# Kernel tuning notes

Measured on AMD Instinct MI355X. Metric: run time of the kernel, lower is better.

## Reference

```python
import jax, jax.numpy as jnp
import numpy as np

TAU_PLUS = 0.02
TAU_MINUS = 0.02
TAU_X = 0.101
A_TRIPLET = 0.0065
HOMEOSTATIC_RATE = 0.1
DT = 0.001
SPIKE_P = 0.05  # spike probability used to binarize inputs


def setup_inputs() -> dict:
    key = jax.random.key(0)
    k1, k2, k3 = jax.random.split(key, 3)
    B, P, Q, T = 16, 2048, 2048, 256
    pre_spikes = (jax.random.uniform(k1, (B, P, T)) < SPIKE_P).astype(jnp.float32)
    post_spikes = (jax.random.uniform(k2, (B, Q, T)) < SPIKE_P).astype(jnp.float32)
    weights = jax.random.normal(k3, (P, Q), dtype=jnp.float32) * 0.1
    meta_A_plus = jnp.float32(0.01)
    meta_A_minus = jnp.float32(0.012)
    return {"pre_spikes": pre_spikes, "post_spikes": post_spikes,
            "weights": weights, "meta_A_plus": meta_A_plus,
            "meta_A_minus": meta_A_minus}


def _traces(spikes_tbn, decay):
    """Trace value used at step t: x_t = decay * (x_{t-1} + s_{t-1}), x_0 = 0."""
    def step(carry, s):
        x = decay * carry          # decayed trace, used for this step's update
        return x + s, x            # spike added AFTER the update, per original
    init = jnp.zeros(spikes_tbn.shape[1:], spikes_tbn.dtype)
    _, xs = jax.lax.scan(step, init, spikes_tbn)
    return xs  # [T, B, N]


def reference(pre_spikes, post_spikes, weights, meta_A_plus, meta_A_minus):
    B, P, T = pre_spikes.shape
    exp_plus = jnp.exp(jnp.float32(-DT / TAU_PLUS))
    exp_minus = jnp.exp(jnp.float32(-DT / TAU_MINUS))
    exp_x = jnp.exp(jnp.float32(-DT / TAU_X))

    pre_t = jnp.transpose(pre_spikes, (2, 0, 1))    # [T, B, P]
    post_t = jnp.transpose(post_spikes, (2, 0, 1))  # [T, B, Q]

    x_pre = _traces(pre_t, exp_plus)     # [T, B, P]
    x_post = _traces(post_t, exp_minus)  # [T, B, Q]
    x_trip = _traces(post_t, exp_x)      # [T, B, Q]

    # Per-step outer products summed over time == one big contraction over (t, b).
    ltp = jnp.einsum('tbp,tbq->pq', x_pre, post_t) * meta_A_plus
    triplet = jnp.einsum('tbp,tbq->pq', x_pre, post_t * x_trip) * A_TRIPLET
    ltd = jnp.einsum('tbp,tbq->pq', pre_t, x_post) * meta_A_minus
    weight_updates = ltp + triplet - ltd

    # Homeostatic scaling (fresh module: activity history holds only this sample)
    current_activity = (pre_spikes.sum() + post_spikes.sum()) / (B * T)
    scaling_factor = jnp.sqrt(HOMEOSTATIC_RATE / (current_activity + 1e-6))

    updated_weights = weights + weight_updates * scaling_factor
    return jnp.clip(updated_weights, -2.0, 2.0)
```

## Files before the change

### kernel.cpp

```cpp
#include <hip/hip_runtime.h>

constexpr int TB = 16;
constexpr int NP = 2048;
constexpr int NQ = 2048;
constexpr int TT = 256;
constexpr int KH = TB * TT;
constexpr int KT = 2 * KH;

typedef unsigned short ushort_t;
typedef __attribute__((ext_vector_type(8))) __bf16 bf16x8;
typedef __attribute__((ext_vector_type(4))) float f32x4;

__device__ __forceinline__ ushort_t f2bf(float f) {
    unsigned u = __builtin_bit_cast(unsigned, f);
    u = (u + 0x7FFFu + ((u >> 16) & 1u)) >> 16;
    return (ushort_t)u;
}

union Pack16 { ushort_t u[16]; uint4 v[2]; };

constexpr float DF1 = 0.95122942450071400910f;
constexpr float DF2 = DF1 * DF1;
constexpr float DF4 = DF2 * DF2;
constexpr float DF8 = DF4 * DF4;
constexpr float DF16 = DF8 * DF8;
constexpr float DF32 = DF16 * DF16;
constexpr float DF64 = DF32 * DF32;
constexpr float DF128 = DF64 * DF64;

constexpr float DX1 = 0.99014786386058731819f;
constexpr float DX2 = DX1 * DX1;
constexpr float DX4 = DX2 * DX2;
constexpr float DX8 = DX4 * DX4;
constexpr float DX16 = DX8 * DX8;
constexpr float DX32 = DX16 * DX16;
constexpr float DX64 = DX32 * DX32;
constexpr float DX128 = DX64 * DX64;

template <int K>
__device__ __forceinline__ float seg_step(float b, float pw, int sl) {
    float t = __shfl_up(b, K, 64);
    return (sl >= K) ? fmaf(pw, t, b) : b;
}

__global__ __launch_bounds__(256, 1) void stage_traces(
    const float* __restrict__ pre, const float* __restrict__ post,
    const float* __restrict__ mApP, const float* __restrict__ mAmP,
    ushort_t* __restrict__ Ab, ushort_t* __restrict__ Bb,
    float* __restrict__ partials)
{
    const int tid  = threadIdx.x;
    const int lane = tid & 63;
    const int wv   = tid >> 6;
    const int sl   = lane & 15;
    const int seg  = lane >> 4;
    const int rowg = blockIdx.x * 16 + wv * 4 + seg;
    const bool isPre = rowg < TB * NP;
    const int m = isPre ? rowg : rowg - TB * NP;
    const int b = m >> 11;
    const int r = m & 2047;

    const float4* src = (const float4*)((isPre ? pre : post) + (size_t)m * TT);
    float f[16];
    #pragma unroll
    for (int j = 0; j < 4; ++j) {
        float4 u = src[sl * 4 + j];
        f[4 * j] = u.x; f[4 * j + 1] = u.y; f[4 * j + 2] = u.z; f[4 * j + 3] = u.w;
    }
    float cnt = 0.f;
    #pragma unroll
    for (int j = 0; j < 16; ++j) cnt += f[j];

    float Cf = 0.f;
    #pragma unroll
    for (int j = 0; j < 16; ++j) Cf = DF1 * (Cf + f[j]);
    float bs = Cf;
    bs = seg_step<1>(bs, DF16, sl);
    bs = seg_step<2>(bs, DF32, sl);
    bs = seg_step<4>(bs, DF64, sl);
    bs = seg_step<8>(bs, DF128, sl);
    float xinf = __shfl_up(bs, 1, 64);
    if (sl == 0) xinf = 0.f;

    float xf[16];
    {
        float x = xinf;
        #pragma unroll
        for (int j = 0; j < 16; ++j) { xf[j] = x; x = DF1 * (x + f[j]); }
    }

    Pack16 pa, pb;
    if (isPre) {
        #pragma unroll
        for (int j = 0; j < 16; ++j) {
            pa.u[j] = f2bf(xf[j]);
            pb.u[j] = (f[j] != 0.f) ? 0x3F80u : 0u;
        }
    } else {
        float Cx = 0.f;
        #pragma unroll
        for (int j = 0; j < 16; ++j) Cx = DX1 * (Cx + f[j]);
        float bx = Cx;
        bx = seg_step<1>(bx, DX16, sl);
        bx = seg_step<2>(bx, DX32, sl);
        bx = seg_step<4>(bx, DX64, sl);
        bx = seg_step<8>(bx, DX128, sl);
        float xint = __shfl_up(bx, 1, 64);
        if (sl == 0) xint = 0.f;

        const float Ap = *mApP;
        const float Am = *mAmP;
        float xt = xint;
        #pragma unroll
        for (int j = 0; j < 16; ++j) {
            pa.u[j] = (f[j] != 0.f) ? f2bf(fmaf(0.0065f, xt, Ap)) : 0u;
            pb.u[j] = f2bf(-Am * xf[j]);
            xt = DX1 * (xt + f[j]);
        }
    }

    ushort_t* o0 = (isPre ? Ab : Bb) + (size_t)r * KT + b * TT + sl * 16;
    *(uint4*)o0       = pa.v[0];
    *(uint4*)(o0 + 8) = pa.v[1];
    *(uint4*)(o0 + KH)     = pb.v[0];
    *(uint4*)(o0 + KH + 8) = pb.v[1];

    #pragma unroll
    for (int off = 32; off > 0; off >>= 1)
        cnt += __shfl_down(cnt, off, 64);
    __shared__ float wsum[4];
    if (lane == 0) wsum[wv] = cnt;
    __syncthreads();
    if (tid == 0) {
        float s = (wsum[0] + wsum[1]) + (wsum[2] + wsum[3]);
        atomicAdd(&partials[(blockIdx.x & 63) * 16], s);
    }
}

__device__ __forceinline__ void async16(const ushort_t* g, ushort_t* l) {
    __builtin_amdgcn_global_load_lds(
        (const __attribute__((address_space(1))) unsigned int*)g,
        (__attribute__((address_space(3))) unsigned int*)l,
        16, 0, 0);
}

__global__ __launch_bounds__(256, 2) void gemm_split(
    const ushort_t* __restrict__ Ab, const ushort_t* __restrict__ Bb,
    float* __restrict__ P0, float* __restrict__ P1)
{
    __shared__ ushort_t As[2][128 * 64];
    __shared__ ushort_t Bs[2][128 * 64];

    const int tid  = threadIdx.x;
    const int lane = tid & 63;
    const int wv   = tid >> 6;
    const int wr   = wv >> 1;
    const int wc   = wv & 1;
    const int quad = lane >> 4;
    const int m16  = lane & 15;

    const int p0 = blockIdx.y * 128;
    const int q0 = blockIdx.x * 128;
    const int kbase = blockIdx.z * (KT / 2);
    const int ldsbase = wv * 512;

    const ushort_t* gaP[4];
    const ushort_t* gbP[4];
    #pragma unroll
    for (int rr = 0; rr < 4; ++rr) {
        const int c   = rr * 256 + tid;
        const int row = c >> 3;
        const int kk8 = (c & 7) ^ (row & 7);
        gaP[rr] = Ab + (size_t)(p0 + row) * KT + kbase + kk8 * 8;
        gbP[rr] = Bb + (size_t)(q0 + row) * KT + kbase + kk8 * 8;
    }

    f32x4 acc[4][4] = {};

    auto stageF = [&](int buf) {
        #pragma unroll
        for (int rr = 0; rr < 4; ++rr) {
            async16(gaP[rr], &As[buf][rr * 2048 + ldsbase]);
            async16(gbP[rr], &Bs[buf][rr * 2048 + ldsbase]);
            gaP[rr] += 64;
            gbP[rr] += 64;
        }
    };
    auto computeF = [&](int buf) {
        #pragma unroll
        for (int ks = 0; ks < 2; ++ks) {
            bf16x8 af[4], bf[4];
            #pragma unroll
            for (int i = 0; i < 4; ++i) {
                const int row  = wr * 64 + i * 16 + m16;
                const int slot = (ks * 4 + quad) ^ (row & 7);
                af[i] = *(const bf16x8*)&As[buf][row * 64 + slot * 8];
            }
            #pragma unroll
            for (int j = 0; j < 4; ++j) {
                const int row  = wc * 64 + j * 16 + m16;
                const int slot = (ks * 4 + quad) ^ (row & 7);
                bf[j] = *(const bf16x8*)&Bs[buf][row * 64 + slot * 8];
            }
            #pragma unroll
            for (int i = 0; i < 4; ++i)
                #pragma unroll
                for (int j = 0; j < 4; ++j)
                    acc[i][j] = __builtin_amdgcn_mfma_f32_16x16x32_bf16(
                        af[i], bf[j], acc[i][j], 0, 0, 0);
        }
    };

    constexpr int NIT = (KT / 2) / 64;
    stageF(0);
    for (int kt2 = 0; kt2 < NIT / 2; ++kt2) {
        __syncthreads();
        stageF(1);
        computeF(0);
        __syncthreads();
        if (kt2 + 1 < NIT / 2)
            stageF(0);
        computeF(1);
    }

    float* P = blockIdx.z ? P1 : P0;
    #pragma unroll
    for (int i = 0; i < 4; ++i) {
        const int prow = p0 + wr * 64 + i * 16 + quad * 4;
        #pragma unroll
        for (int j = 0; j < 4; ++j) {
            const int qcol = q0 + wc * 64 + j * 16 + m16;
            #pragma unroll
            for (int r2 = 0; r2 < 4; ++r2)
                P[(size_t)(prow + r2) * NQ + qcol] = acc[i][j][r2];
        }
    }
}

__global__ __launch_bounds__(256) void merge_out(
    const float* __restrict__ W, const float* __restrict__ P1,
    const float* __restrict__ partials, float* __restrict__ Out)
{
    __shared__ float s_scale;
    const int tid = threadIdx.x;
    if (tid < 64) {
        float v = partials[tid * 16];
        #pragma unroll
        for (int off = 32; off > 0; off >>= 1)
            v += __shfl_down(v, off, 64);
        if (tid == 0)
            s_scale = sqrtf(0.1f / (v * (1.0f / 4096.0f) + 1e-6f));
    }
    __syncthreads();
    const float scale = s_scale;

    const size_t i4 = (size_t)blockIdx.x * 256 + tid;
    float4 w = ((const float4*)W)[i4];
    float4 a = ((const float4*)Out)[i4];
    float4 c = ((const float4*)P1)[i4];
    float4 o;
    o.x = fminf(fmaxf(fmaf(scale, a.x + c.x, w.x), -2.f), 2.f);
    o.y = fminf(fmaxf(fmaf(scale, a.y + c.y, w.y), -2.f), 2.f);
    o.z = fminf(fmaxf(fmaf(scale, a.z + c.z, w.z), -2.f), 2.f);
    o.w = fminf(fmaxf(fmaf(scale, a.w + c.w, w.w), -2.f), 2.f);
    ((float4*)Out)[i4] = o;
}

extern "C" void kernel_launch(void* const* d_in, const int* in_sizes, int n_in,
                              void* d_out, int out_size, void* d_ws, size_t ws_size,
                              hipStream_t stream) {
    const float* pre  = (const float*)d_in[0];
    const float* post = (const float*)d_in[1];
    const float* W    = (const float*)d_in[2];
    const float* mAp  = (const float*)d_in[3];
    const float* mAm  = (const float*)d_in[4];
    float* out = (float*)d_out;

    char* ws = (char*)d_ws;
    float* partials = (float*)ws;
    ushort_t* Ab = (ushort_t*)(ws + 16384);
    ushort_t* Bb = (ushort_t*)(ws + 16384 + (size_t)NP * KT * 2);
    float* P1    = (float*)(ws + 16384 + 2 * (size_t)NP * KT * 2);

    hipMemsetAsync(partials, 0, 64 * 16 * sizeof(float), stream);

    stage_traces<<<dim3((TB * NP + TB * NQ) / 16), dim3(256), 0, stream>>>(
        pre, post, mAp, mAm, Ab, Bb, partials);

    gemm_split<<<dim3(NQ / 128, NP / 128, 2), dim3(256), 0, stream>>>(
        Ab, Bb, out, P1);

    merge_out<<<dim3(NP * NQ / 1024), dim3(256), 0, stream>>>(
        W, P1, partials, out);
}
```

Measured before the change: 208.6 us.

## Remap GEMM blocks to XCD-local tile groups and streamline trace staging registers

The GEMM launch changes from a 3D grid to a flat 512-block grid, and block IDs are remapped so that blocks landing on the same XCD (id & 7) share a 4x8 group of output tiles. Such blocks reuse the same A and B rows in that XCD's L2. The trace staging kernel is also rewritten to keep spike data in float4 registers and pack bf16 pairs directly instead of going through a ushort union array, and its launch bound no longer forces one block per SM. The remap relies on the hardware dispatching blocks round-robin across XCDs.

```diff
diff --git a/kernel.cpp b/kernel.cpp
--- a/kernel.cpp
+++ b/kernel.cpp
@@ -11,13 +11,16 @@
 typedef __attribute__((ext_vector_type(8))) __bf16 bf16x8;
 typedef __attribute__((ext_vector_type(4))) float f32x4;
 
-__device__ __forceinline__ ushort_t f2bf(float f) {
+__device__ __forceinline__ unsigned bf1(float f) {
     unsigned u = __builtin_bit_cast(unsigned, f);
-    u = (u + 0x7FFFu + ((u >> 16) & 1u)) >> 16;
-    return (ushort_t)u;
-}
-
-union Pack16 { ushort_t u[16]; uint4 v[2]; };
+    return (u + 0x7FFFu + ((u >> 16) & 1u)) >> 16;
+}
+__device__ __forceinline__ unsigned pack2(float lo, float hi) {
+    return bf1(lo) | (bf1(hi) << 16);
+}
+__device__ __forceinline__ unsigned spk2(float a, float b) {
+    return ((a != 0.f) ? 0x3F80u : 0u) | ((b != 0.f) ? 0x3F800000u : 0u);
+}
 
 constexpr float DF1 = 0.95122942450071400910f;
 constexpr float DF2 = DF1 * DF1;
@@ -43,7 +46,20 @@
     return (sl >= K) ? fmaf(pw, t, b) : b;
 }
 
-__global__ __launch_bounds__(256, 1) void stage_traces(
+__device__ __forceinline__ float fold4(float C, float4 u, float d) {
+    C = d * (C + u.x); C = d * (C + u.y); C = d * (C + u.z); C = d * (C + u.w);
+    return C;
+}
+__device__ __forceinline__ float4 expand4(float& x, float4 u, float d) {
+    float4 t;
+    t.x = x; x = d * (x + u.x);
+    t.y = x; x = d * (x + u.y);
+    t.z = x; x = d * (x + u.z);
+    t.w = x; x = d * (x + u.w);
+    return t;
+}
+
+__global__ __launch_bounds__(256) void stage_traces(
     const float* __restrict__ pre, const float* __restrict__ post,
     const float* __restrict__ mApP, const float* __restrict__ mAmP,
     ushort_t* __restrict__ Ab, ushort_t* __restrict__ Bb,
@@ -60,20 +76,14 @@
     const int b = m >> 11;
     const int r = m & 2047;
 
-    const float4* src = (const float4*)((isPre ? pre : post) + (size_t)m * TT);
-    float f[16];
-    #pragma unroll
-    for (int j = 0; j < 4; ++j) {
-        float4 u = src[sl * 4 + j];
-        f[4 * j] = u.x; f[4 * j + 1] = u.y; f[4 * j + 2] = u.z; f[4 * j + 3] = u.w;
-    }
-    float cnt = 0.f;
-    #pragma unroll
-    for (int j = 0; j < 16; ++j) cnt += f[j];
-
-    float Cf = 0.f;
-    #pragma unroll
-    for (int j = 0; j < 16; ++j) Cf = DF1 * (Cf + f[j]);
+    const float4* src =
+        (const float4*)((isPre ? pre : post) + (size_t)m * TT) + sl * 4;
+    const float4 u0 = src[0], u1 = src[1], u2 = src[2], u3 = src[3];
+
+    float cnt = ((u0.x + u0.y) + (u0.z + u0.w)) + ((u1.x + u1.y) + (u1.z + u1.w))
+              + ((u2.x + u2.y) + (u2.z + u2.w)) + ((u3.x + u3.y) + (u3.z + u3.w));
+
+    float Cf = fold4(fold4(fold4(fold4(0.f, u0, DF1), u1, DF1), u2, DF1), u3, DF1);
     float bs = Cf;
     bs = seg_step<1>(bs, DF16, sl);
     bs = seg_step<2>(bs, DF32, sl);
@@ -82,24 +92,24 @@
     float xinf = __shfl_up(bs, 1, 64);
     if (sl == 0) xinf = 0.f;
 
-    float xf[16];
-    {
-        float x = xinf;
-        #pragma unroll
-        for (int j = 0; j < 16; ++j) { xf[j] = x; x = DF1 * (x + f[j]); }
-    }
-
-    Pack16 pa, pb;
+    float xm = xinf;
+    const float4 t0 = expand4(xm, u0, DF1);
+    const float4 t1 = expand4(xm, u1, DF1);
+    const float4 t2 = expand4(xm, u2, DF1);
+    const float4 t3 = expand4(xm, u3, DF1);
+
+    uint4 va, va2, vb, vb2;
     if (isPre) {
-        #pragma unroll
-        for (int j = 0; j < 16; ++j) {
-            pa.u[j] = f2bf(xf[j]);
-            pb.u[j] = (f[j] != 0.f) ? 0x3F80u : 0u;
-        }
+        va  = uint4{pack2(t0.x, t0.y), pack2(t0.z, t0.w),
+                    pack2(t1.x, t1.y), pack2(t1.z, t1.w)};
+        va2 = uint4{pack2(t2.x, t2.y), pack2(t2.z, t2.w),
+                    pack2(t3.x, t3.y), pack2(t3.z, t3.w)};
+        vb  = uint4{spk2(u0.x, u0.y), spk2(u0.z, u0.w),
+                    spk2(u1.x, u1.y), spk2(u1.z, u1.w)};
+        vb2 = uint4{spk2(u2.x, u2.y), spk2(u2.z, u2.w),
+                    spk2(u3.x, u3.y), spk2(u3.z, u3.w)};
     } else {
-        float Cx = 0.f;
-        #pragma unroll
-        for (int j = 0; j < 16; ++j) Cx = DX1 * (Cx + f[j]);
+        float Cx = fold4(fold4(fold4(fold4(0.f, u0, DX1), u1, DX1), u2, DX1), u3, DX1);
         float bx = Cx;
         bx = seg_step<1>(bx, DX16, sl);
         bx = seg_step<2>(bx, DX32, sl);
@@ -108,22 +118,34 @@
         float xint = __shfl_up(bx, 1, 64);
         if (sl == 0) xint = 0.f;
 
+        float xt = xint;
+        const float4 w0 = expand4(xt, u0, DX1);
+        const float4 w1 = expand4(xt, u1, DX1);
+        const float4 w2 = expand4(xt, u2, DX1);
+        const float4 w3 = expand4(xt, u3, DX1);
+
         const float Ap = *mApP;
         const float Am = *mAmP;
-        float xt = xint;
-        #pragma unroll
-        for (int j = 0; j < 16; ++j) {
-            pa.u[j] = (f[j] != 0.f) ? f2bf(fmaf(0.0065f, xt, Ap)) : 0u;
-            pb.u[j] = f2bf(-Am * xf[j]);
-            xt = DX1 * (xt + f[j]);
-        }
+        auto av2 = [&](float sa, float ta, float sb, float tb) -> unsigned {
+            unsigned lo = (sa != 0.f) ? bf1(fmaf(0.0065f, ta, Ap)) : 0u;
+            unsigned hi = (sb != 0.f) ? bf1(fmaf(0.0065f, tb, Ap)) : 0u;
+            return lo | (hi << 16);
+        };
+        va  = uint4{av2(u0.x, w0.x, u0.y, w0.y), av2(u0.z, w0.z, u0.w, w0.w),
+                    av2(u1.x, w1.x, u1.y, w1.y), av2(u1.z, w1.z, u1.w, w1.w)};
+        va2 = uint4{av2(u2.x, w2.x, u2.y, w2.y), av2(u2.z, w2.z, u2.w, w2.w),
+                    av2(u3.x, w3.x, u3.y, w3.y), av2(u3.z, w3.z, u3.w, w3.w)};
+        vb  = uint4{pack2(-Am * t0.x, -Am * t0.y), pack2(-Am * t0.z, -Am * t0.w),
+                    pack2(-Am * t1.x, -Am * t1.y), pack2(-Am * t1.z, -Am * t1.w)};
+        vb2 = uint4{pack2(-Am * t2.x, -Am * t2.y), pack2(-Am * t2.z, -Am * t2.w),
+                    pack2(-Am * t3.x, -Am * t3.y), pack2(-Am * t3.z, -Am * t3.w)};
     }
 
     ushort_t* o0 = (isPre ? Ab : Bb) + (size_t)r * KT + b * TT + sl * 16;
-    *(uint4*)o0       = pa.v[0];
-    *(uint4*)(o0 + 8) = pa.v[1];
-    *(uint4*)(o0 + KH)     = pb.v[0];
-    *(uint4*)(o0 + KH + 8) = pb.v[1];
+    ((uint4*)o0)[0] = va;
+    ((uint4*)o0)[1] = va2;
+    ((uint4*)(o0 + KH))[0] = vb;
+    ((uint4*)(o0 + KH))[1] = vb2;
 
     #pragma unroll
     for (int off = 32; off > 0; off >>= 1)
@@ -159,9 +181,17 @@
     const int quad = lane >> 4;
     const int m16  = lane & 15;
 
-    const int p0 = blockIdx.y * 128;
-    const int q0 = blockIdx.x * 128;
-    const int kbase = blockIdx.z * (KT / 2);
+    const int id  = blockIdx.x;
+    const int xcd = id & 7;
+    const int j5  = id >> 3;
+    const int z   = j5 & 1;
+    const int t   = j5 >> 1;
+    const int pt  = ((xcd >> 1) << 2) + (t >> 3);
+    const int qt  = ((xcd & 1) << 3) + (t & 7);
+
+    const int p0 = pt * 128;
+    const int q0 = qt * 128;
+    const int kbase = z * (KT / 2);
     const int ldsbase = wv * 512;
 
     const ushort_t* gaP[4];
@@ -197,17 +227,17 @@
                 af[i] = *(const bf16x8*)&As[buf][row * 64 + slot * 8];
             }
             #pragma unroll
-            for (int j = 0; j < 4; ++j) {
-                const int row  = wc * 64 + j * 16 + m16;
+            for (int jj = 0; jj < 4; ++jj) {
+                const int row  = wc * 64 + jj * 16 + m16;
                 const int slot = (ks * 4 + quad) ^ (row & 7);
-                bf[j] = *(const bf16x8*)&Bs[buf][row * 64 + slot * 8];
+                bf[jj] = *(const bf16x8*)&Bs[buf][row * 64 + slot * 8];
             }
             #pragma unroll
             for (int i = 0; i < 4; ++i)
                 #pragma unroll
-                for (int j = 0; j < 4; ++j)
-                    acc[i][j] = __builtin_amdgcn_mfma_f32_16x16x32_bf16(
-                        af[i], bf[j], acc[i][j], 0, 0, 0);
+                for (int jj = 0; jj < 4; ++jj)
+                    acc[i][jj] = __builtin_amdgcn_mfma_f32_16x16x32_bf16(
+                        af[i], bf[jj], acc[i][jj], 0, 0, 0);
         }
     };
 
@@ -223,16 +253,16 @@
         computeF(1);
     }
 
-    float* P = blockIdx.z ? P1 : P0;
+    float* P = z ? P1 : P0;
     #pragma unroll
     for (int i = 0; i < 4; ++i) {
         const int prow = p0 + wr * 64 + i * 16 + quad * 4;
         #pragma unroll
-        for (int j = 0; j < 4; ++j) {
-            const int qcol = q0 + wc * 64 + j * 16 + m16;
+        for (int jj = 0; jj < 4; ++jj) {
+            const int qcol = q0 + wc * 64 + jj * 16 + m16;
             #pragma unroll
             for (int r2 = 0; r2 < 4; ++r2)
-                P[(size_t)(prow + r2) * NQ + qcol] = acc[i][j][r2];
+                P[(size_t)(prow + r2) * NQ + qcol] = acc[i][jj][r2];
         }
     }
 }
@@ -287,8 +317,7 @@
     stage_traces<<<dim3((TB * NP + TB * NQ) / 16), dim3(256), 0, stream>>>(
         pre, post, mAp, mAm, Ab, Bb, partials);
 
-    gemm_split<<<dim3(NQ / 128, NP / 128, 2), dim3(256), 0, stream>>>(
-        Ab, Bb, out, P1);
+    gemm_split<<<dim3(512), dim3(256), 0, stream>>>(Ab, Bb, out, P1);
 
     merge_out<<<dim3(NP * NQ / 1024), dim3(256), 0, stream>>>(
         W, P1, partials, out);
```

Measured after the change: 205.9 us. No clear change (-1.3%).
